# Kernel optimization log

Hardware: AMD Instinct MI355X
Metric: run time of the kernel (lower is better)

The kernel has to match this reference:

```python
import jax, jax.numpy as jnp
import numpy as np

B, T, D, H = 4, 1024, 1024, 16  # batch, seq, model dim (named head_size in source), n_heads


def setup_inputs() -> dict:
    key = jax.random.key(0)
    ks = jax.random.split(key, 12)
    s = 0.02
    x = jax.random.normal(ks[0], (B, T, D), jnp.float32)
    x1 = jax.random.normal(ks[1], (1,), jnp.float32)  # unused by module
    x2 = jax.random.normal(ks[2], (1,), jnp.float32)  # unused by module
    # bool mask, True = masked out; causal upper-triangular as typical usage
    attn_mask = jnp.triu(jnp.ones((T, T), dtype=bool), k=1)
    Wk = jax.random.normal(ks[3], (D, D), jnp.float32) * s
    bk = jax.random.normal(ks[4], (D,), jnp.float32) * s
    Wq = jax.random.normal(ks[5], (D, D), jnp.float32) * s
    bq = jax.random.normal(ks[6], (D,), jnp.float32) * s
    Wv = jax.random.normal(ks[7], (D, D), jnp.float32) * s
    bv = jax.random.normal(ks[8], (D,), jnp.float32) * s
    Wp = jax.random.normal(ks[9], (D, D), jnp.float32) * s
    bp = jax.random.normal(ks[10], (D,), jnp.float32) * s
    return {"x": x, "x1": x1, "x2": x2, "attn_mask": attn_mask,
            "Wk": Wk, "bk": bk, "Wq": Wq, "bq": bq,
            "Wv": Wv, "bv": bv, "Wp": Wp, "bp": bp}


def reference(x, x1, x2, attn_mask, Wk, bk, Wq, bq, Wv, bv, Wp, bp):
    b, t, c = x.shape
    n_heads = H
    hd = c // n_heads
    # torch nn.Linear: y = x @ W.T + b
    k = (x @ Wk.T + bk).reshape(b, t, n_heads, hd)
    q = (x @ Wq.T + bq).reshape(b, t, n_heads, hd)
    v = (x @ Wv.T + bv).reshape(b, t, n_heads, hd)
    scores = jnp.einsum('bkhi,bqhi->bkqh', k, q)  # [B,T(k),T(q),H]
    # mask BEFORE scaling (as in source; -inf is scale-invariant)
    scores = jnp.where(attn_mask[None, :t, :t, None], -jnp.inf, scores)
    scores = scores / jnp.sqrt(jnp.asarray(c, scores.dtype))  # scale by full model dim (source quirk)
    weights = jax.nn.softmax(scores, axis=2)  # softmax over QUERY axis (source quirk)
    out = jnp.einsum('bkqh,bqhj->bkhj', weights, v).reshape(b, t, c)
    out = out @ Wp.T + bp  # dropout p=0 -> identity
    return (out, weights)
```

## Files before the change

kernel.cpp:

```cpp
#include <hip/hip_runtime.h>
#include <cstdint>


typedef __bf16 bf16x8 __attribute__((ext_vector_type(8)));
typedef float  f32x4  __attribute__((ext_vector_type(4)));
using u16 = unsigned short;
using u32 = unsigned int;

__device__ __forceinline__ float bf2f(u16 u) {
  union { u32 u; float f; } x; x.u = ((u32)u) << 16; return x.f;
}
__device__ __forceinline__ u16 f2bf(float f) {
  union { float f; u32 u; } x; x.f = f;
  u32 u = x.u;
  return (u16)((u + 0x7fffu + ((u >> 16) & 1u)) >> 16);
}

__device__ __forceinline__ void storeC(float* p, float v) { *p = v; }
__device__ __forceinline__ void storeC(u16* p, float v)   { *p = f2bf(v); }

#define GLL(g, s) __builtin_amdgcn_global_load_lds(                      \
    (const __attribute__((address_space(1))) u32*)(g),                   \
    (__attribute__((address_space(3))) u32*)(s), 16, 0, 0)

__global__ __launch_bounds__(256) void cvt_all(const float4* __restrict__ x,
                                               const float4* __restrict__ wk,
                                               const float4* __restrict__ wq,
                                               const float4* __restrict__ wv,
                                               const float4* __restrict__ wp,
                                               uint2* __restrict__ out) {
  int i = blockIdx.x * 256 + threadIdx.x;
  const float4* src; int off;
  if (i < 1048576) { src = x; off = i; }
  else {
    int j = i - 1048576; int w = j >> 18; off = j & 262143;
    src = (w == 0) ? wk : (w == 1) ? wq : (w == 2) ? wv : wp;
  }
  float4 v = src[off];
  uint2 o;
  o.x = (u32)f2bf(v.x) | ((u32)f2bf(v.y) << 16);
  o.y = (u32)f2bf(v.z) | ((u32)f2bf(v.w) << 16);
  out[i] = o;
}

__global__ __launch_bounds__(256) void pack_bias(const float* __restrict__ b0,
                                                 const float* __restrict__ b1,
                                                 const float* __restrict__ b2,
                                                 float* __restrict__ out) {
  int t = blockIdx.x * 256 + threadIdx.x;
  const float* src = (t < 1024) ? b0 : (t < 2048) ? b1 : b2;
  out[t] = src[t & 1023];
}

template <typename CT>
__global__ __launch_bounds__(256) void gemm_nt(
    const u16* __restrict__ A, const u16* __restrict__ B,
    const float* __restrict__ bias, CT* __restrict__ C,
    int M, int N, int K, int lda, int ldb, int ldc,
    int nH, long long sAb, long long sAh, long long sBb, long long sBh,
    long long sCb, long long sCh, float alpha, int biasStrideH)
{
  const int m0 = blockIdx.y * 128;
  const int n0 = blockIdx.x * 128;

  int z = blockIdx.z;
  int bb = z / nH, hh = z % nH;
  A += bb * sAb + hh * sAh;
  B += bb * sBb + hh * sBh;
  C += bb * sCb + hh * sCh;

  __shared__ __align__(16) u16 As[128 * 32];
  __shared__ __align__(16) u16 Bs[128 * 32];

  const int t    = threadIdx.x;
  const int wave = t >> 6;
  const int lane = t & 63;

  const int r0 = (wave * 2 + 0) * 16 + (lane >> 2);
  const int r1 = (wave * 2 + 1) * 16 + (lane >> 2);
  const int cl = (lane & 3) * 8;
  const u16* aG0 = A + (size_t)(m0 + r0) * lda + cl;
  const u16* aG1 = A + (size_t)(m0 + r1) * lda + cl;
  const u16* bG0 = B + (size_t)(n0 + r0) * ldb + cl;
  const u16* bG1 = B + (size_t)(n0 + r1) * ldb + cl;
  u16* asD0 = As + (wave * 2 + 0) * 512;
  u16* asD1 = As + (wave * 2 + 1) * 512;
  u16* bsD0 = Bs + (wave * 2 + 0) * 512;
  u16* bsD1 = Bs + (wave * 2 + 1) * 512;

  const int wm = (wave >> 1) << 6;
  const int wn = (wave & 1) << 6;
  const int lr = lane & 15;
  const int lk = (lane >> 4) << 3;

  f32x4 acc[4][4];
  const f32x4 fzero = {0.f, 0.f, 0.f, 0.f};
#pragma unroll
  for (int i = 0; i < 4; i++)
#pragma unroll
    for (int j = 0; j < 4; j++) acc[i][j] = fzero;

  for (int k0 = 0; k0 < K; k0 += 32) {
    __syncthreads();
    GLL(aG0 + k0, asD0);
    GLL(aG1 + k0, asD1);
    GLL(bG0 + k0, bsD0);
    GLL(bG1 + k0, bsD1);
    __syncthreads();

    bf16x8 af[4], bf[4];
#pragma unroll
    for (int mi = 0; mi < 4; mi++)
      af[mi] = *(const bf16x8*)&As[(wm + mi * 16 + lr) * 32 + lk];
#pragma unroll
    for (int ni = 0; ni < 4; ni++)
      bf[ni] = *(const bf16x8*)&Bs[(wn + ni * 16 + lr) * 32 + lk];
#pragma unroll
    for (int mi = 0; mi < 4; mi++)
#pragma unroll
      for (int ni = 0; ni < 4; ni++)
        acc[mi][ni] = __builtin_amdgcn_mfma_f32_16x16x32_bf16(af[mi], bf[ni], acc[mi][ni], 0, 0, 0);
  }

  const int cr = (lane >> 4) << 2;
  const int cc = lane & 15;
#pragma unroll
  for (int mi = 0; mi < 4; mi++) {
#pragma unroll
    for (int ni = 0; ni < 4; ni++) {
      int gn = n0 + wn + ni * 16 + cc;
      if (gn >= N) continue;
      float bv = bias ? bias[biasStrideH * hh + gn] : 0.f;
      int gm = m0 + wm + mi * 16 + cr;
#pragma unroll
      for (int r = 0; r < 4; r++) {
        float v = acc[mi][ni][r] * alpha + bv;
        storeC(&C[(size_t)(gm + r) * ldc + gn], v);
      }
    }
  }
}

__global__ __launch_bounds__(256) void transpose_v(const u16* __restrict__ v, u16* __restrict__ vt) {
  __shared__ u16 tile[32][33];
  int z = blockIdx.z;
  int b = z >> 4, h = z & 15;
  int q0 = blockIdx.x * 32;
  int j0 = blockIdx.y * 32;
  int tx = threadIdx.x;
  int ty = threadIdx.y;
#pragma unroll
  for (int i = 0; i < 4; i++) {
    int r = ty + i * 8;
    tile[r][tx] = v[(size_t)(b * 1024 + q0 + r) * 1024 + h * 64 + j0 + tx];
  }
  __syncthreads();
#pragma unroll
  for (int i = 0; i < 4; i++) {
    int r = ty + i * 8;
    vt[(size_t)(z * 64 + j0 + r) * 1024 + q0 + tx] = tile[tx][r];
  }
}

__global__ __launch_bounds__(256, 2) void fused_attn(
    const u16* __restrict__ kq,
    const u16* __restrict__ vt,
    u16* __restrict__ sc, u16* __restrict__ attn, float* __restrict__ lbuf)
{
  const int kb = 7 - blockIdx.x;
  const int bh = blockIdx.y;
  const int b  = bh >> 4, h = bh & 15;
  const int k0 = kb << 7;

  __shared__ __align__(16) u16 Kl[128 * 72];
  __shared__ __align__(16) u16 QV[128 * 72];
  __shared__ __align__(16) u16 Pl[128 * 136];
  __shared__ float l_sm[2][128];

  const int t    = threadIdx.x;
  const int wave = t >> 6, lane = t & 63;
  const int wm = (wave >> 1) << 6, wn = (wave & 1) << 6;
  const int lr = lane & 15, lk = (lane >> 4) << 3;
  const int cr = (lane >> 4) << 2, cc = lane & 15;

  {
    const int r = t >> 1, cb = (t & 1) << 5;
    const u16* g = kq + (size_t)(b * 1024 + k0 + r) * 1024 + h * 64 + cb;
    u16* d = Kl + r * 72 + cb;
#pragma unroll
    for (int i = 0; i < 4; i++)
      *(uint4*)(d + i * 8) = *(const uint4*)(g + i * 8);
  }

  const u16* qbase = kq + 4194304 + (size_t)(b * 1024) * 1024 + h * 64;
  const u16* vbase = vt + (size_t)(bh * 64) * 1024;

  f32x4 oacc[2][4];
  const f32x4 fz = {0.f, 0.f, 0.f, 0.f};
#pragma unroll
  for (int i = 0; i < 2; i++)
#pragma unroll
    for (int j = 0; j < 4; j++) oacc[i][j] = fz;
  float lsum[4][4] = {};

  const int qr = t >> 1, qcb = (t & 1) << 5;
  const int vr = t >> 2, vcb = (t & 3) << 5;

  for (int tq = 0; tq <= kb; tq++) {
    const int q0 = tq << 7;
    uint4 qreg[4], vreg[4];
    const u16* qg = qbase + (size_t)(q0 + qr) * 1024 + qcb;
    const u16* vg = vbase + (size_t)vr * 1024 + q0 + vcb;
#pragma unroll
    for (int i = 0; i < 4; i++) qreg[i] = *(const uint4*)(qg + i * 8);
#pragma unroll
    for (int i = 0; i < 4; i++) vreg[i] = *(const uint4*)(vg + i * 8);

    __syncthreads();
    {
      u16* d = QV + qr * 72 + qcb;
#pragma unroll
      for (int i = 0; i < 4; i++) *(uint4*)(d + i * 8) = qreg[i];
    }
    __syncthreads();

    f32x4 sacc[4][4];
#pragma unroll
    for (int i = 0; i < 4; i++)
#pragma unroll
      for (int j = 0; j < 4; j++) sacc[i][j] = fz;
#pragma unroll
    for (int ks = 0; ks < 2; ks++) {
      bf16x8 af[4], bf[4];
#pragma unroll
      for (int mi = 0; mi < 4; mi++)
        af[mi] = *(const bf16x8*)&Kl[(wm + mi * 16 + lr) * 72 + ks * 32 + lk];
#pragma unroll
      for (int ni = 0; ni < 4; ni++)
        bf[ni] = *(const bf16x8*)&QV[(wn + ni * 16 + lr) * 72 + ks * 32 + lk];
#pragma unroll
      for (int mi = 0; mi < 4; mi++)
#pragma unroll
        for (int ni = 0; ni < 4; ni++)
          sacc[mi][ni] = __builtin_amdgcn_mfma_f32_16x16x32_bf16(af[mi], bf[ni], sacc[mi][ni], 0, 0, 0);
    }
    __syncthreads();

#pragma unroll
    for (int mi = 0; mi < 4; mi++) {
#pragma unroll
      for (int ni = 0; ni < 4; ni++) {
        const int col = wn + ni * 16 + cc;
#pragma unroll
        for (int r = 0; r < 4; r++) {
          const int row = wm + mi * 16 + cr + r;
          bool valid = (q0 + col) <= (k0 + row);
          float e = valid ? __expf(sacc[mi][ni][r] * 0.03125f) : 0.f;
          lsum[mi][r] += e;
          u32 bb = f2bf(e);
          u32 ob = (u32)__shfl_xor((int)bb, 1, 64);
          if ((lane & 1) == 0)
            *(u32*)&Pl[row * 136 + (col & ~1)] = bb | (ob << 16);
        }
      }
    }
    {
      u16* d = QV + vr * 136 + vcb;
#pragma unroll
      for (int i = 0; i < 4; i++) *(uint4*)(d + i * 8) = vreg[i];
    }
    __syncthreads();

#pragma unroll
    for (int ks = 0; ks < 4; ks++) {
      bf16x8 pa[2], vb[4];
#pragma unroll
      for (int mi = 0; mi < 2; mi++)
        pa[mi] = *(const bf16x8*)&Pl[(wave * 32 + mi * 16 + lr) * 136 + ks * 32 + lk];
#pragma unroll
      for (int ni = 0; ni < 4; ni++)
        vb[ni] = *(const bf16x8*)&QV[(ni * 16 + lr) * 136 + ks * 32 + lk];
#pragma unroll
      for (int mi = 0; mi < 2; mi++)
#pragma unroll
        for (int ni = 0; ni < 4; ni++)
          oacc[mi][ni] = __builtin_amdgcn_mfma_f32_16x16x32_bf16(pa[mi], vb[ni], oacc[mi][ni], 0, 0, 0);
    }
    {
      const int r = t >> 1, cb2 = (t & 1) << 6;
      u16* g = sc + ((size_t)bh << 20) + (size_t)(k0 + r) * 1024 + q0 + cb2;
      const u16* s = Pl + r * 136 + cb2;
#pragma unroll
      for (int i = 0; i < 8; i++) *(uint4*)(g + i * 8) = *(const uint4*)(s + i * 8);
    }
  }

#pragma unroll
  for (int mi = 0; mi < 4; mi++)
#pragma unroll
    for (int r = 0; r < 4; r++) {
      float v = lsum[mi][r];
#pragma unroll
      for (int o = 1; o < 16; o <<= 1) v += __shfl_xor(v, o, 64);
      lsum[mi][r] = v;
    }
  __syncthreads();
  if ((lane & 15) == 0) {
#pragma unroll
    for (int mi = 0; mi < 4; mi++)
#pragma unroll
      for (int r = 0; r < 4; r++)
        l_sm[wave & 1][wm + mi * 16 + cr + r] = lsum[mi][r];
  }
  __syncthreads();
  if (t < 128)
    lbuf[(size_t)bh * 1024 + k0 + t] = l_sm[0][t] + l_sm[1][t];

#pragma unroll
  for (int mi = 0; mi < 2; mi++) {
#pragma unroll
    for (int r = 0; r < 4; r++) {
      const int row = wave * 32 + mi * 16 + cr + r;
      const float rinv = 1.f / (l_sm[0][row] + l_sm[1][row]);
#pragma unroll
      for (int ni = 0; ni < 4; ni++)
        attn[(size_t)(b * 1024 + k0 + row) * 1024 + h * 64 + ni * 16 + cc] =
            f2bf(oacc[mi][ni][r] * rinv);
    }
  }
}

__global__ __launch_bounds__(1024) void expand_norm(const u16* __restrict__ sw,
                                                    const float* __restrict__ lbuf,
                                                    float* __restrict__ out_w) {
  __shared__ u32 lds[16 * 576];

  const int bk   = blockIdx.x;
  const int b    = bk >> 10, k = bk & 1023;
  const int w    = threadIdx.x >> 6;
  const int lane = threadIdx.x & 63;
  const int qb   = lane << 4;

  const float rinv = 1.f / lbuf[(size_t)(b * 16 + w) * 1024 + k];
  const u16* row = sw + (((size_t)(b * 16 + w)) << 20) + ((size_t)k << 10);

  union { uint4 d; u16 s[8]; } a0, a1;
  if (qb <= k) {
    a0.d = *(const uint4*)(row + qb);
    a1.d = *(const uint4*)(row + qb + 8);
  } else {
    a0.d = make_uint4(0, 0, 0, 0);
    a1.d = make_uint4(0, 0, 0, 0);
  }

  u16 outp[16];
#pragma unroll
  for (int j = 0; j < 16; j++) {
    u16 raw = (j < 8) ? a0.s[j] : a1.s[j - 8];
    float e = ((qb + j) <= k) ? bf2f(raw) * rinv : 0.f;
    outp[j] = f2bf(e);
  }

  u32* run = &lds[w * 576 + lane * 9];
#pragma unroll
  for (int j = 0; j < 8; j++) run[j] = (u32)outp[2 * j] | ((u32)outp[2 * j + 1] << 16);
  __syncthreads();

  const int t    = threadIdx.x;
  const int Lr   = t >> 4;
  const int pr   = (t & 15) >> 1;
  const int half = (t & 1) << 4;

  float vals[16];
#pragma unroll
  for (int h = 0; h < 16; h++) {
    u32 packed = lds[h * 576 + Lr * 9 + pr];
    vals[h] = bf2f((u16)(packed >> half));
  }

  float4* o = (float4*)(out_w + (((size_t)bk << 10) + t) * 16);
  o[0] = make_float4(vals[0],  vals[1],  vals[2],  vals[3]);
  o[1] = make_float4(vals[4],  vals[5],  vals[6],  vals[7]);
  o[2] = make_float4(vals[8],  vals[9],  vals[10], vals[11]);
  o[3] = make_float4(vals[12], vals[13], vals[14], vals[15]);
}

extern "C" void kernel_launch(void* const* d_in, const int* in_sizes, int n_in,
                              void* d_out, int out_size, void* d_ws, size_t ws_size,
                              hipStream_t stream) {
  const float* x  = (const float*)d_in[0];
  const float* Wk = (const float*)d_in[4];
  const float* bk = (const float*)d_in[5];
  const float* Wq = (const float*)d_in[6];
  const float* bq = (const float*)d_in[7];
  const float* Wv = (const float*)d_in[8];
  const float* bv = (const float*)d_in[9];
  const float* Wp = (const float*)d_in[10];
  const float* bp = (const float*)d_in[11];

  float* out   = (float*)d_out;
  float* out_w = out + 4194304;

  u16* ws   = (u16*)d_ws;
  u16* xb   = ws;
  u16* wkb  = xb  + 4194304;
  u16* kbuf = wkb + 4194304;
  u16* vbuf = kbuf + 8388608;
  u16* vt   = kbuf + 12582912;
  u16* attn = vt   + 4194304;
  u16* sc   = attn + 4194304;
  float* bqkv = (float*)(sc + 67108864);
  float* lbuf = bqkv + 3072;

  cvt_all<<<8192, 256, 0, stream>>>((const float4*)x, (const float4*)Wk, (const float4*)Wq,
                                    (const float4*)Wv, (const float4*)Wp, (uint2*)ws);
  pack_bias<<<12, 256, 0, stream>>>(bk, bq, bv, bqkv);

  gemm_nt<u16><<<dim3(8, 32, 3), 256, 0, stream>>>(
      xb, wkb, bqkv, kbuf, 4096, 1024, 1024, 1024, 1024, 1024,
      3, 0, 0, 0, 1048576, 0, 4194304, 1.0f, 1024);

  transpose_v<<<dim3(32, 2, 64), dim3(32, 8), 0, stream>>>(vbuf, vt);

  fused_attn<<<dim3(8, 64), 256, 0, stream>>>(kbuf, vt, sc, attn, lbuf);

  expand_norm<<<4096, 1024, 0, stream>>>(sc, lbuf, out_w);

  gemm_nt<float><<<dim3(8, 32, 1), 256, 0, stream>>>(
      attn, wkb + 3145728, bp, out, 4096, 1024, 1024, 1024, 1024, 1024,
      1, 0, 0, 0, 0, 0, 0, 1.0f, 0);
}
```

Baseline: 548.3 us.

## Fuse V transpose into QKV GEMM, merge bias packing, and rework score/weight stores

```diff
diff --git a/kernel.cpp b/kernel.cpp
--- a/kernel.cpp
+++ b/kernel.cpp
@@ -28,7 +28,16 @@
                                                const float4* __restrict__ wq,
                                                const float4* __restrict__ wv,
                                                const float4* __restrict__ wp,
-                                               uint2* __restrict__ out) {
+                                               uint2* __restrict__ out,
+                                               const float* __restrict__ bkp,
+                                               const float* __restrict__ bqp,
+                                               float* __restrict__ bqkv) {
+  if (blockIdx.x >= 8192) {
+    int t2 = (blockIdx.x - 8192) * 256 + threadIdx.x;
+    const float* s = (t2 < 1024) ? bkp : bqp;
+    bqkv[t2] = s[t2 & 1023];
+    return;
+  }
   int i = blockIdx.x * 256 + threadIdx.x;
   const float4* src; int off;
   if (i < 1048576) { src = x; off = i; }
@@ -43,13 +52,95 @@
   out[i] = o;
 }
 
-__global__ __launch_bounds__(256) void pack_bias(const float* __restrict__ b0,
-                                                 const float* __restrict__ b1,
-                                                 const float* __restrict__ b2,
-                                                 float* __restrict__ out) {
-  int t = blockIdx.x * 256 + threadIdx.x;
-  const float* src = (t < 1024) ? b0 : (t < 2048) ? b1 : b2;
-  out[t] = src[t & 1023];
+__global__ __launch_bounds__(256) void gemm_qkvt(
+    const u16* __restrict__ xb, const u16* __restrict__ wkb,
+    const float* __restrict__ bkq, const float* __restrict__ bv,
+    u16* __restrict__ kq, u16* __restrict__ vt)
+{
+  const int z  = blockIdx.z;
+  const int n0 = blockIdx.x * 128;
+  const u16 *A, *B; u16* C; const float* bias;
+  int m0; bool rowBias;
+  if (z < 2) {
+    m0 = blockIdx.y * 128;
+    A = xb; B = wkb + z * 1048576; C = kq + (size_t)z * 4194304;
+    bias = bkq + z * 1024; rowBias = false;
+  } else {
+    const int b = blockIdx.y >> 3;
+    m0 = (blockIdx.y & 7) * 128;
+    A = wkb + 2 * 1048576; B = xb + (size_t)b * 1048576; C = vt + (size_t)b * 1048576;
+    bias = bv; rowBias = true;
+  }
+
+  __shared__ __align__(16) u16 As[128 * 32];
+  __shared__ __align__(16) u16 Bs[128 * 32];
+
+  const int t    = threadIdx.x;
+  const int wave = t >> 6;
+  const int lane = t & 63;
+
+  const int r0 = (wave * 2 + 0) * 16 + (lane >> 2);
+  const int r1 = (wave * 2 + 1) * 16 + (lane >> 2);
+  const int cl = (lane & 3) * 8;
+  const u16* aG0 = A + (size_t)(m0 + r0) * 1024 + cl;
+  const u16* aG1 = A + (size_t)(m0 + r1) * 1024 + cl;
+  const u16* bG0 = B + (size_t)(n0 + r0) * 1024 + cl;
+  const u16* bG1 = B + (size_t)(n0 + r1) * 1024 + cl;
+  u16* asD0 = As + (wave * 2 + 0) * 512;
+  u16* asD1 = As + (wave * 2 + 1) * 512;
+  u16* bsD0 = Bs + (wave * 2 + 0) * 512;
+  u16* bsD1 = Bs + (wave * 2 + 1) * 512;
+
+  const int wm = (wave >> 1) << 6;
+  const int wn = (wave & 1) << 6;
+  const int lr = lane & 15;
+  const int lk = (lane >> 4) << 3;
+
+  f32x4 acc[4][4];
+  const f32x4 fzero = {0.f, 0.f, 0.f, 0.f};
+#pragma unroll
+  for (int i = 0; i < 4; i++)
+#pragma unroll
+    for (int j = 0; j < 4; j++) acc[i][j] = fzero;
+
+  for (int k0 = 0; k0 < 1024; k0 += 32) {
+    __syncthreads();
+    GLL(aG0 + k0, asD0);
+    GLL(aG1 + k0, asD1);
+    GLL(bG0 + k0, bsD0);
+    GLL(bG1 + k0, bsD1);
+    __syncthreads();
+
+    bf16x8 af[4], bf[4];
+#pragma unroll
+    for (int mi = 0; mi < 4; mi++)
+      af[mi] = *(const bf16x8*)&As[(wm + mi * 16 + lr) * 32 + lk];
+#pragma unroll
+    for (int ni = 0; ni < 4; ni++)
+      bf[ni] = *(const bf16x8*)&Bs[(wn + ni * 16 + lr) * 32 + lk];
+#pragma unroll
+    for (int mi = 0; mi < 4; mi++)
+#pragma unroll
+      for (int ni = 0; ni < 4; ni++)
+        acc[mi][ni] = __builtin_amdgcn_mfma_f32_16x16x32_bf16(af[mi], bf[ni], acc[mi][ni], 0, 0, 0);
+  }
+
+  const int cr = (lane >> 4) << 2;
+  const int cc = lane & 15;
+#pragma unroll
+  for (int mi = 0; mi < 4; mi++) {
+#pragma unroll
+    for (int ni = 0; ni < 4; ni++) {
+      int gn = n0 + wn + ni * 16 + cc;
+      float bcol = rowBias ? 0.f : bias[gn];
+      int gm = m0 + wm + mi * 16 + cr;
+#pragma unroll
+      for (int r = 0; r < 4; r++) {
+        float badd = rowBias ? bias[gm + r] : bcol;
+        C[(size_t)(gm + r) * 1024 + gn] = f2bf(acc[mi][ni][r] + badd);
+      }
+    }
+  }
 }
 
 template <typename CT>
@@ -141,27 +232,6 @@
   }
 }
 
-__global__ __launch_bounds__(256) void transpose_v(const u16* __restrict__ v, u16* __restrict__ vt) {
-  __shared__ u16 tile[32][33];
-  int z = blockIdx.z;
-  int b = z >> 4, h = z & 15;
-  int q0 = blockIdx.x * 32;
-  int j0 = blockIdx.y * 32;
-  int tx = threadIdx.x;
-  int ty = threadIdx.y;
-#pragma unroll
-  for (int i = 0; i < 4; i++) {
-    int r = ty + i * 8;
-    tile[r][tx] = v[(size_t)(b * 1024 + q0 + r) * 1024 + h * 64 + j0 + tx];
-  }
-  __syncthreads();
-#pragma unroll
-  for (int i = 0; i < 4; i++) {
-    int r = ty + i * 8;
-    vt[(size_t)(z * 64 + j0 + r) * 1024 + q0 + tx] = tile[tx][r];
-  }
-}
-
 __global__ __launch_bounds__(256, 2) void fused_attn(
     const u16* __restrict__ kq,
     const u16* __restrict__ vt,
@@ -287,11 +357,12 @@
           oacc[mi][ni] = __builtin_amdgcn_mfma_f32_16x16x32_bf16(pa[mi], vb[ni], oacc[mi][ni], 0, 0, 0);
     }
     {
-      const int r = t >> 1, cb2 = (t & 1) << 6;
-      u16* g = sc + ((size_t)bh << 20) + (size_t)(k0 + r) * 1024 + q0 + cb2;
-      const u16* s = Pl + r * 136 + cb2;
-#pragma unroll
-      for (int i = 0; i < 8; i++) *(uint4*)(g + i * 8) = *(const uint4*)(s + i * 8);
+      const int rr = t >> 4, cp = (t & 15) << 3;
+      u16* g = sc + ((size_t)bh << 20) + (size_t)(k0 + rr) * 1024 + q0 + cp;
+      const u16* s = Pl + rr * 136 + cp;
+#pragma unroll
+      for (int i = 0; i < 8; i++)
+        *(uint4*)(g + (size_t)(i * 16) * 1024) = *(const uint4*)(s + i * 16 * 136);
     }
   }
 
@@ -333,7 +404,7 @@
 __global__ __launch_bounds__(1024) void expand_norm(const u16* __restrict__ sw,
                                                     const float* __restrict__ lbuf,
                                                     float* __restrict__ out_w) {
-  __shared__ u32 lds[16 * 576];
+  __shared__ u32 lds[16 * 577];
 
   const int bk   = blockIdx.x;
   const int b    = bk >> 10, k = bk & 1023;
@@ -361,28 +432,28 @@
     outp[j] = f2bf(e);
   }
 
-  u32* run = &lds[w * 576 + lane * 9];
+  u32* run = &lds[w * 577 + lane * 9];
 #pragma unroll
   for (int j = 0; j < 8; j++) run[j] = (u32)outp[2 * j] | ((u32)outp[2 * j + 1] << 16);
   __syncthreads();
 
-  const int t    = threadIdx.x;
-  const int Lr   = t >> 4;
-  const int pr   = (t & 15) >> 1;
-  const int half = (t & 1) << 4;
-
-  float vals[16];
-#pragma unroll
-  for (int h = 0; h < 16; h++) {
-    u32 packed = lds[h * 576 + Lr * 9 + pr];
-    vals[h] = bf2f((u16)(packed >> half));
-  }
-
-  float4* o = (float4*)(out_w + (((size_t)bk << 10) + t) * 16);
-  o[0] = make_float4(vals[0],  vals[1],  vals[2],  vals[3]);
-  o[1] = make_float4(vals[4],  vals[5],  vals[6],  vals[7]);
-  o[2] = make_float4(vals[8],  vals[9],  vals[10], vals[11]);
-  o[3] = make_float4(vals[12], vals[13], vals[14], vals[15]);
+  const int t = threadIdx.x;
+  f32x4* o = (f32x4*)(out_w + ((size_t)bk << 14));
+#pragma unroll
+  for (int p = 0; p < 4; p++) {
+    const int q    = p * 256 + (t >> 2);
+    const int Lr   = q >> 4;
+    const int pr   = (q & 15) >> 1;
+    const int half = (q & 1) << 4;
+    f32x4 v;
+#pragma unroll
+    for (int j = 0; j < 4; j++) {
+      const int hh = (t & 3) * 4 + j;
+      u32 packed = lds[hh * 577 + Lr * 9 + pr];
+      v[j] = bf2f((u16)(packed >> half));
+    }
+    __builtin_nontemporal_store(v, o + p * 1024 + t);
+  }
 }
 
 extern "C" void kernel_launch(void* const* d_in, const int* in_sizes, int n_in,
@@ -405,22 +476,17 @@
   u16* xb   = ws;
   u16* wkb  = xb  + 4194304;
   u16* kbuf = wkb + 4194304;
-  u16* vbuf = kbuf + 8388608;
   u16* vt   = kbuf + 12582912;
   u16* attn = vt   + 4194304;
   u16* sc   = attn + 4194304;
   float* bqkv = (float*)(sc + 67108864);
   float* lbuf = bqkv + 3072;
 
-  cvt_all<<<8192, 256, 0, stream>>>((const float4*)x, (const float4*)Wk, (const float4*)Wq,
-                                    (const float4*)Wv, (const float4*)Wp, (uint2*)ws);
-  pack_bias<<<12, 256, 0, stream>>>(bk, bq, bv, bqkv);
-
-  gemm_nt<u16><<<dim3(8, 32, 3), 256, 0, stream>>>(
-      xb, wkb, bqkv, kbuf, 4096, 1024, 1024, 1024, 1024, 1024,
-      3, 0, 0, 0, 1048576, 0, 4194304, 1.0f, 1024);
-
-  transpose_v<<<dim3(32, 2, 64), dim3(32, 8), 0, stream>>>(vbuf, vt);
+  cvt_all<<<8200, 256, 0, stream>>>((const float4*)x, (const float4*)Wk, (const float4*)Wq,
+                                    (const float4*)Wv, (const float4*)Wp, (uint2*)ws,
+                                    bk, bq, bqkv);
+
+  gemm_qkvt<<<dim3(8, 32, 3), 256, 0, stream>>>(xb, wkb, bqkv, bv, kbuf, vt);
 
   fused_attn<<<dim3(8, 64), 256, 0, stream>>>(kbuf, vt, sc, attn, lbuf);
 
```

After: 473.4 us. 1.16x faster.
